# Kernel optimization log

Measured on AMD Instinct MI355X. Metric: run time of the kernel, lower is better.

## Reference

```python
import jax, jax.numpy as jnp
import numpy as np

N = 100_000      # nodes
E = 1_600_000    # edges
B = 256          # graphs
DIM = 64
EPS = 1e-5


def _batchnorm(h, gamma, beta):
    # BatchNorm1d in training mode: batch mean, biased variance
    mu = jnp.mean(h, axis=0)
    var = jnp.mean((h - mu) ** 2, axis=0)
    return (h - mu) * jax.lax.rsqrt(var + EPS) * gamma + beta


def setup_inputs() -> dict:
    key = jax.random.key(0)
    ks = jax.random.split(key, 12)
    x = jax.random.normal(ks[0], (N, DIM), dtype=jnp.float32)
    edge_index = jax.random.randint(ks[1], (2, E), 0, N, dtype=jnp.int64)
    edge_attr = jax.random.normal(ks[2], (E, DIM), dtype=jnp.float32)
    state = jax.random.normal(ks[3], (B, DIM), dtype=jnp.float32)
    batch = jnp.sort(jax.random.randint(ks[4], (N,), 0, B, dtype=jnp.int64))
    s = 0.05
    params = {
        "W1": jax.random.normal(ks[5], (DIM, 3 * DIM), dtype=jnp.float32) * s,
        "b1": jnp.zeros((DIM,), jnp.float32),
        "g1": jnp.ones((DIM,), jnp.float32),
        "be1": jnp.zeros((DIM,), jnp.float32),
        "W2": jax.random.normal(ks[6], (DIM, DIM), dtype=jnp.float32) * s,
        "b2": jnp.zeros((DIM,), jnp.float32),
        "g2": jnp.ones((DIM,), jnp.float32),
        "be2": jnp.zeros((DIM,), jnp.float32),
        "W3": jax.random.normal(ks[7], (DIM, DIM), dtype=jnp.float32) * s,
        "b3": jnp.zeros((DIM,), jnp.float32),
        "g3": jnp.ones((DIM,), jnp.float32),
        "be3": jnp.zeros((DIM,), jnp.float32),
    }
    return {"x": x, "edge_index": edge_index, "edge_attr": edge_attr,
            "state": state, "batch": batch, **params}


def reference(x, edge_index, edge_attr, state, batch,
              W1, b1, g1, be1, W2, b2, g2, be2, W3, b3, g3, be3):
    n = x.shape[0]
    src = edge_index[0]
    # scatter-mean of edge_attr onto destination-of-src nodes
    sums = jax.ops.segment_sum(edge_attr, src, num_segments=n)
    cnt = jax.ops.segment_sum(jnp.ones((edge_attr.shape[0],), edge_attr.dtype),
                              src, num_segments=n)
    v_mean = sums / jnp.maximum(cnt, 1.0)[:, None]
    comb = jnp.concatenate([x, v_mean, state[batch]], axis=1)  # [N, 3*DIM]
    h = jax.nn.relu(comb @ W1.T + b1)
    h = _batchnorm(h, g1, be1)
    h = jax.nn.relu(h @ W2.T + b2)
    h = _batchnorm(h, g2, be2)
    h = h @ W3.T + b3
    return _batchnorm(h, g3, be3)
```

## Files before the change

### kernel.cpp

```cpp
#include <hip/hip_runtime.h>

#define NN 100000
#define NE 1600000
#define EPSV 1e-5f

typedef float f32x4 __attribute__((ext_vector_type(4)));
typedef short s16x8 __attribute__((ext_vector_type(8)));

__device__ __forceinline__ unsigned short f2bf(float f) {
  unsigned int u = __float_as_uint(f);
  u += 0x7fffu + ((u >> 16) & 1u);
  return (unsigned short)(u >> 16);
}

__device__ __forceinline__ ushort4 pack4(float4 v) {
  ushort4 s;
  s.x = f2bf(v.x); s.y = f2bf(v.y); s.z = f2bf(v.z); s.w = f2bf(v.w);
  return s;
}

__global__ __launch_bounds__(256) void k_bucket(
    const int* __restrict__ ei, int* __restrict__ cnt, int* __restrict__ eids) {
  int e = blockIdx.x * 256 + threadIdx.x;
  int src = ei[e];
  int pos = atomicAdd(&cnt[src], 1);
  if (pos < 64) eids[(size_t)src * 64 + pos] = e;
}

__global__ __launch_bounds__(256) void k_gather(
    const int* __restrict__ cnt, const int* __restrict__ eids,
    const float* __restrict__ ea, float* __restrict__ vmean) {
  int n = __builtin_amdgcn_readfirstlane(blockIdx.x * 4 + (threadIdx.x >> 6));
  int lane = threadIdx.x & 63;
  const int* elist = eids + (size_t)n * 64;
  int c = cnt[n];
  int m = c < 64 ? c : 64;
  float a0 = 0.f, a1 = 0.f, a2 = 0.f, a3 = 0.f;
  int e = 0;
  for (; e + 4 <= m; e += 4) {
    int i0 = elist[e], i1 = elist[e + 1], i2 = elist[e + 2], i3 = elist[e + 3];
    a0 += ea[(size_t)i0 * 64 + lane];
    a1 += ea[(size_t)i1 * 64 + lane];
    a2 += ea[(size_t)i2 * 64 + lane];
    a3 += ea[(size_t)i3 * 64 + lane];
  }
  for (; e < m; ++e) a0 += ea[(size_t)elist[e] * 64 + lane];
  float inv = 1.0f / fmaxf((float)c, 1.0f);
  vmean[(size_t)n * 64 + lane] = (a0 + a1 + a2 + a3) * inv;
}

__global__ __launch_bounds__(256) void k_g1(
    const float4* __restrict__ x4, const float4* __restrict__ vmean4,
    const float4* __restrict__ state4,
    const int* __restrict__ batch, const float4* __restrict__ w14,
    const float* __restrict__ b1, unsigned short* __restrict__ h1,
    float* __restrict__ Sout, float* __restrict__ Qout) {
  __shared__ unsigned short lc[64][200];
  __shared__ unsigned short lw[64][200];
  __shared__ float ssum[64], ssq[64];
  const int tid = threadIdx.x;
  const int nodeBase = blockIdx.x * 64;
  if (tid < 64) { ssum[tid] = 0.f; ssq[tid] = 0.f; }
#pragma unroll
  for (int i = 0; i < 12; ++i) {
    int idx = tid + i * 256;
    int row = idx / 48, q = idx % 48;
    *(ushort4*)&lw[row][q * 4] = pack4(w14[idx]);
  }
#pragma unroll
  for (int i = 0; i < 4; ++i) {
    int idx = tid + i * 256;
    int node = idx >> 4, q = idx & 15;
    int g = nodeBase + node;
    float4 vx = {0,0,0,0}, vm = {0,0,0,0}, vs = {0,0,0,0};
    if (g < NN) {
      vx = x4[(size_t)g * 16 + q];
      vm = vmean4[(size_t)g * 16 + q];
      int b = batch[g];
      vs = state4[b * 16 + q];
    }
    *(ushort4*)&lc[node][q * 4]       = pack4(vx);
    *(ushort4*)&lc[node][64 + q * 4]  = pack4(vm);
    *(ushort4*)&lc[node][128 + q * 4] = pack4(vs);
  }
  __syncthreads();
  const int lane = tid & 63, w = tid >> 6;
  const int rg = lane >> 4, ci = lane & 15;
  f32x4 acc[4] = {{0,0,0,0},{0,0,0,0},{0,0,0,0},{0,0,0,0}};
#pragma unroll
  for (int s = 0; s < 6; ++s) {
    int k0 = 32 * s + rg * 8;
    s16x8 a = *(const s16x8*)&lc[w * 16 + ci][k0];
#pragma unroll
    for (int c = 0; c < 4; ++c) {
      s16x8 b = *(const s16x8*)&lw[c * 16 + ci][k0];
      acc[c] = __builtin_amdgcn_mfma_f32_16x16x32_bf16(a, b, acc[c], 0, 0, 0);
    }
  }
#pragma unroll
  for (int c = 0; c < 4; ++c) {
    int col = c * 16 + ci;
    float bb = b1[col];
    float ls = 0.f, lq = 0.f;
#pragma unroll
    for (int r = 0; r < 4; ++r) {
      int g = nodeBase + w * 16 + rg * 4 + r;
      if (g < NN) {
        float v = fmaxf(acc[c][r] + bb, 0.f);
        h1[(size_t)g * 64 + col] = f2bf(v);
        ls += v; lq += v * v;
      }
    }
    atomicAdd(&ssum[col], ls);
    atomicAdd(&ssq[col], lq);
  }
  __syncthreads();
  if (tid < 64) {
    unsafeAtomicAdd(&Sout[tid], ssum[tid]);
    unsafeAtomicAdd(&Qout[tid], ssq[tid]);
  }
}

template <bool RELU, bool OUTF32>
__global__ __launch_bounds__(256) void k_gemm64(
    const s16x8* __restrict__ A8,
    const float4* __restrict__ w4,
    const float* __restrict__ bias,
    const float* __restrict__ gm, const float* __restrict__ bt,
    const float* __restrict__ Sin, const float* __restrict__ Qin,
    unsigned short* __restrict__ Obf, float* __restrict__ Of32,
    float* __restrict__ Sout, float* __restrict__ Qout) {
  __shared__ unsigned short la[64][72];
  __shared__ unsigned short lwf[64][72];
  __shared__ float lA[64], lC[64], lD[64], ssum[64], ssq[64];
  const int tid = threadIdx.x;
  const int nodeBase = blockIdx.x * 64;
  if (tid < 64) {
    float mu = Sin[tid] * (1.0f / NN);
    float var = Qin[tid] * (1.0f / NN) - mu * mu;
    float a = gm[tid] * rsqrtf(var + EPSV);
    lA[tid] = a;
    lC[tid] = bt[tid] - mu * a;
    ssum[tid] = 0.f; ssq[tid] = 0.f;
  }
  __syncthreads();
#pragma unroll
  for (int i = 0; i < 2; ++i) {
    int idx = tid + i * 256;
    int row = idx >> 3, q = idx & 7;
    int g = nodeBase + row;
    s16x8 v = {};
    if (g < NN) v = A8[(size_t)g * 8 + q];
    *(s16x8*)&la[row][q * 8] = v;
  }
#pragma unroll
  for (int i = 0; i < 4; ++i) {
    int idx = tid + i * 256;
    int j = idx >> 4, q = idx & 15;
    float4 v = w4[idx];
    int k = q * 4;
    ushort4 s;
    s.x = f2bf(v.x * lA[k]);     s.y = f2bf(v.y * lA[k + 1]);
    s.z = f2bf(v.z * lA[k + 2]); s.w = f2bf(v.w * lA[k + 3]);
    *(ushort4*)&lwf[j][k] = s;
  }
  if (tid < 64) {
    const float* W = (const float*)w4 + tid * 64;
    float d = bias[tid];
    for (int k = 0; k < 64; ++k) d += lC[k] * W[k];
    lD[tid] = d;
  }
  __syncthreads();
  const int lane = tid & 63, w = tid >> 6;
  const int rg = lane >> 4, ci = lane & 15;
  f32x4 acc[4] = {{0,0,0,0},{0,0,0,0},{0,0,0,0},{0,0,0,0}};
#pragma unroll
  for (int s = 0; s < 2; ++s) {
    int k0 = 32 * s + rg * 8;
    s16x8 a = *(const s16x8*)&la[w * 16 + ci][k0];
#pragma unroll
    for (int c = 0; c < 4; ++c) {
      s16x8 b = *(const s16x8*)&lwf[c * 16 + ci][k0];
      acc[c] = __builtin_amdgcn_mfma_f32_16x16x32_bf16(a, b, acc[c], 0, 0, 0);
    }
  }
#pragma unroll
  for (int c = 0; c < 4; ++c) {
    int col = c * 16 + ci;
    float dd = lD[col];
    float ls = 0.f, lq = 0.f;
#pragma unroll
    for (int r = 0; r < 4; ++r) {
      int g = nodeBase + w * 16 + rg * 4 + r;
      if (g < NN) {
        float v = acc[c][r] + dd;
        if (RELU) v = fmaxf(v, 0.f);
        if (OUTF32) Of32[(size_t)g * 64 + col] = v;
        else        Obf[(size_t)g * 64 + col] = f2bf(v);
        ls += v; lq += v * v;
      }
    }
    atomicAdd(&ssum[col], ls);
    atomicAdd(&ssq[col], lq);
  }
  __syncthreads();
  if (tid < 64) {
    unsafeAtomicAdd(&Sout[tid], ssum[tid]);
    unsafeAtomicAdd(&Qout[tid], ssq[tid]);
  }
}

__global__ __launch_bounds__(256) void k_bn3(
    const float4* __restrict__ h3, const float* __restrict__ gm,
    const float* __restrict__ bt, const float* __restrict__ S,
    const float* __restrict__ Q, float4* __restrict__ out) {
  __shared__ float lA[64], lC[64];
  const int tid = threadIdx.x;
  if (tid < 64) {
    float mu = S[tid] * (1.0f / NN);
    float var = Q[tid] * (1.0f / NN) - mu * mu;
    float a = gm[tid] * rsqrtf(var + EPSV);
    lA[tid] = a;
    lC[tid] = bt[tid] - mu * a;
  }
  __syncthreads();
  const int total = NN * 16;
  for (int idx = blockIdx.x * 256 + tid; idx < total; idx += gridDim.x * 256) {
    float4 v = h3[idx];
    int k = (idx & 15) * 4;
    v.x = v.x * lA[k]     + lC[k];
    v.y = v.y * lA[k + 1] + lC[k + 1];
    v.z = v.z * lA[k + 2] + lC[k + 2];
    v.w = v.w * lA[k + 3] + lC[k + 3];
    out[idx] = v;
  }
}

extern "C" void kernel_launch(void* const* d_in, const int* in_sizes, int n_in,
                              void* d_out, int out_size, void* d_ws, size_t ws_size,
                              hipStream_t stream) {
  const float* x     = (const float*)d_in[0];
  const int*   ei    = (const int*)d_in[1];
  const float* ea    = (const float*)d_in[2];
  const float* state = (const float*)d_in[3];
  const int*   batch = (const int*)d_in[4];
  const float* W1  = (const float*)d_in[5];
  const float* b1  = (const float*)d_in[6];
  const float* g1  = (const float*)d_in[7];
  const float* be1 = (const float*)d_in[8];
  const float* W2  = (const float*)d_in[9];
  const float* b2  = (const float*)d_in[10];
  const float* g2  = (const float*)d_in[11];
  const float* be2 = (const float*)d_in[12];
  const float* W3  = (const float*)d_in[13];
  const float* b3  = (const float*)d_in[14];
  const float* g3  = (const float*)d_in[15];
  const float* be3 = (const float*)d_in[16];

  char* ws = (char*)d_ws;
  int*   cnt  = (int*)ws;
  float* S1   = (float*)(ws + 400000);
  float* Q1 = S1 + 64;
  float* S2 = S1 + 128;
  float* Q2 = S1 + 192;
  float* S3 = S1 + 256;
  float* Q3 = S1 + 320;
  int*            eids  = (int*)(ws + 401536);
  float*          h3    = (float*)(ws + 401536);
  float*          vmean = (float*)(ws + 26001536);
  unsigned short* h2    = (unsigned short*)(ws + 26001536);
  unsigned short* h1    = (unsigned short*)(ws + 51601536);

  hipMemsetAsync(ws, 0, 401536, stream);

  k_bucket<<<NE / 256, 256, 0, stream>>>(ei, cnt, eids);
  k_gather<<<NN / 4, 256, 0, stream>>>(cnt, eids, ea, vmean);

  const int nblk = (NN + 63) / 64;
  k_g1<<<nblk, 256, 0, stream>>>((const float4*)x, (const float4*)vmean,
                                 (const float4*)state, batch, (const float4*)W1,
                                 b1, h1, S1, Q1);
  k_gemm64<true, false><<<nblk, 256, 0, stream>>>(
      (const s16x8*)h1, (const float4*)W2, b2, g1, be1, S1, Q1, h2, nullptr, S2, Q2);
  k_gemm64<false, true><<<nblk, 256, 0, stream>>>(
      (const s16x8*)h2, (const float4*)W3, b3, g2, be2, S2, Q2, nullptr, h3, S3, Q3);
  k_bn3<<<2048, 256, 0, stream>>>((const float4*)h3, g3, be3, S3, Q3, (float4*)d_out);
}
```

Measured before the change: 399.5 us.

## Vectorize gather, store intermediates as bf16, stage outputs in LDS, precompute folded weights

The edge gather now uses float4 loads with four edge groups per wave and a shuffle reduction, and stores the mean in bf16. GEMM outputs go through LDS so global stores are 16-byte coalesced, and h3 is kept in bf16 to halve its traffic. BatchNorm folding of W2/W3 moves into a single-block prep kernel instead of being redone in every block. In exchange there are two extra serial launches and more bf16 rounding in vmean and h3.

```diff
diff --git a/kernel.cpp b/kernel.cpp
--- a/kernel.cpp
+++ b/kernel.cpp
@@ -11,6 +11,10 @@
   unsigned int u = __float_as_uint(f);
   u += 0x7fffu + ((u >> 16) & 1u);
   return (unsigned short)(u >> 16);
+}
+
+__device__ __forceinline__ float bf2f(unsigned short s) {
+  return __uint_as_float(((unsigned int)s) << 16);
 }
 
 __device__ __forceinline__ ushort4 pack4(float4 v) {
@@ -29,28 +33,45 @@
 
 __global__ __launch_bounds__(256) void k_gather(
     const int* __restrict__ cnt, const int* __restrict__ eids,
-    const float* __restrict__ ea, float* __restrict__ vmean) {
+    const float4* __restrict__ ea4, ushort4* __restrict__ vmb4) {
   int n = __builtin_amdgcn_readfirstlane(blockIdx.x * 4 + (threadIdx.x >> 6));
   int lane = threadIdx.x & 63;
+  int grp = lane >> 4, q = lane & 15;
   const int* elist = eids + (size_t)n * 64;
   int c = cnt[n];
   int m = c < 64 ? c : 64;
-  float a0 = 0.f, a1 = 0.f, a2 = 0.f, a3 = 0.f;
-  int e = 0;
-  for (; e + 4 <= m; e += 4) {
-    int i0 = elist[e], i1 = elist[e + 1], i2 = elist[e + 2], i3 = elist[e + 3];
-    a0 += ea[(size_t)i0 * 64 + lane];
-    a1 += ea[(size_t)i1 * 64 + lane];
-    a2 += ea[(size_t)i2 * 64 + lane];
-    a3 += ea[(size_t)i3 * 64 + lane];
-  }
-  for (; e < m; ++e) a0 += ea[(size_t)elist[e] * 64 + lane];
-  float inv = 1.0f / fmaxf((float)c, 1.0f);
-  vmean[(size_t)n * 64 + lane] = (a0 + a1 + a2 + a3) * inv;
+  float ax = 0.f, ay = 0.f, az = 0.f, aw = 0.f;
+  for (int e = 0; e < m; e += 16) {
+    int rm = m - 1;
+    int r0 = e + grp, r1 = e + 4 + grp, r2 = e + 8 + grp, r3 = e + 12 + grp;
+    int i0 = elist[r0 < m ? r0 : rm];
+    int i1 = elist[r1 < m ? r1 : rm];
+    int i2 = elist[r2 < m ? r2 : rm];
+    int i3 = elist[r3 < m ? r3 : rm];
+    float4 v0 = ea4[(size_t)i0 * 16 + q];
+    float4 v1 = ea4[(size_t)i1 * 16 + q];
+    float4 v2 = ea4[(size_t)i2 * 16 + q];
+    float4 v3 = ea4[(size_t)i3 * 16 + q];
+    float m0 = r0 < m ? 1.f : 0.f, m1 = r1 < m ? 1.f : 0.f;
+    float m2 = r2 < m ? 1.f : 0.f, m3 = r3 < m ? 1.f : 0.f;
+    ax += m0 * v0.x + m1 * v1.x + m2 * v2.x + m3 * v3.x;
+    ay += m0 * v0.y + m1 * v1.y + m2 * v2.y + m3 * v3.y;
+    az += m0 * v0.z + m1 * v1.z + m2 * v2.z + m3 * v3.z;
+    aw += m0 * v0.w + m1 * v1.w + m2 * v2.w + m3 * v3.w;
+  }
+  ax += __shfl_xor(ax, 16); ay += __shfl_xor(ay, 16);
+  az += __shfl_xor(az, 16); aw += __shfl_xor(aw, 16);
+  ax += __shfl_xor(ax, 32); ay += __shfl_xor(ay, 32);
+  az += __shfl_xor(az, 32); aw += __shfl_xor(aw, 32);
+  if (lane < 16) {
+    float inv = 1.0f / fmaxf((float)c, 1.0f);
+    float4 r; r.x = ax * inv; r.y = ay * inv; r.z = az * inv; r.w = aw * inv;
+    vmb4[(size_t)n * 16 + lane] = pack4(r);
+  }
 }
 
 __global__ __launch_bounds__(256) void k_g1(
-    const float4* __restrict__ x4, const float4* __restrict__ vmean4,
+    const float4* __restrict__ x4, const ushort4* __restrict__ vmb4,
     const float4* __restrict__ state4,
     const int* __restrict__ batch, const float4* __restrict__ w14,
     const float* __restrict__ b1, unsigned short* __restrict__ h1,
@@ -72,15 +93,16 @@
     int idx = tid + i * 256;
     int node = idx >> 4, q = idx & 15;
     int g = nodeBase + node;
-    float4 vx = {0,0,0,0}, vm = {0,0,0,0}, vs = {0,0,0,0};
+    float4 vx = {0,0,0,0}, vs = {0,0,0,0};
+    ushort4 vm = {0,0,0,0};
     if (g < NN) {
       vx = x4[(size_t)g * 16 + q];
-      vm = vmean4[(size_t)g * 16 + q];
+      vm = vmb4[(size_t)g * 16 + q];
       int b = batch[g];
       vs = state4[b * 16 + q];
     }
     *(ushort4*)&lc[node][q * 4]       = pack4(vx);
-    *(ushort4*)&lc[node][64 + q * 4]  = pack4(vm);
+    *(ushort4*)&lc[node][64 + q * 4]  = vm;
     *(ushort4*)&lc[node][128 + q * 4] = pack4(vs);
   }
   __syncthreads();
@@ -97,6 +119,8 @@
       acc[c] = __builtin_amdgcn_mfma_f32_16x16x32_bf16(a, b, acc[c], 0, 0, 0);
     }
   }
+  __syncthreads();
+  unsigned short (*lo)[72] = (unsigned short(*)[72])lw;
 #pragma unroll
   for (int c = 0; c < 4; ++c) {
     int col = c * 16 + ci;
@@ -104,46 +128,71 @@
     float ls = 0.f, lq = 0.f;
 #pragma unroll
     for (int r = 0; r < 4; ++r) {
-      int g = nodeBase + w * 16 + rg * 4 + r;
-      if (g < NN) {
-        float v = fmaxf(acc[c][r] + bb, 0.f);
-        h1[(size_t)g * 64 + col] = f2bf(v);
-        ls += v; lq += v * v;
-      }
+      int row = w * 16 + rg * 4 + r;
+      float v = fmaxf(acc[c][r] + bb, 0.f);
+      lo[row][col] = f2bf(v);
+      if (nodeBase + row < NN) { ls += v; lq += v * v; }
     }
     atomicAdd(&ssum[col], ls);
     atomicAdd(&ssq[col], lq);
   }
   __syncthreads();
+#pragma unroll
+  for (int i = 0; i < 2; ++i) {
+    int idx = tid + i * 256;
+    int row = idx >> 3, q = idx & 7;
+    int g = nodeBase + row;
+    if (g < NN) *(s16x8*)&h1[(size_t)g * 64 + q * 8] = *(const s16x8*)&lo[row][q * 8];
+  }
   if (tid < 64) {
     unsafeAtomicAdd(&Sout[tid], ssum[tid]);
     unsafeAtomicAdd(&Qout[tid], ssq[tid]);
   }
 }
 
-template <bool RELU, bool OUTF32>
+__global__ __launch_bounds__(256) void k_prep(
+    const float* __restrict__ Sin, const float* __restrict__ Qin,
+    const float* __restrict__ gm, const float* __restrict__ bt,
+    const float* __restrict__ W, const float* __restrict__ bias,
+    unsigned short* __restrict__ wf, float* __restrict__ dout) {
+  __shared__ float lA[64], lC[64], red[256];
+  int t = threadIdx.x;
+  if (t < 64) {
+    float mu = Sin[t] * (1.0f / NN);
+    float var = Qin[t] * (1.0f / NN) - mu * mu;
+    float a = gm[t] * rsqrtf(var + EPSV);
+    lA[t] = a;
+    lC[t] = bt[t] - mu * a;
+  }
+  __syncthreads();
+#pragma unroll
+  for (int i = 0; i < 16; ++i) {
+    int idx = t + i * 256;
+    wf[idx] = f2bf(W[idx] * lA[idx & 63]);
+  }
+  int j = t >> 2, p = t & 3;
+  const float* Wr = W + j * 64 + p * 16;
+  float s = 0.f;
+#pragma unroll
+  for (int k = 0; k < 16; ++k) s += lC[p * 16 + k] * Wr[k];
+  red[t] = s;
+  __syncthreads();
+  if (t < 64) dout[t] = bias[t] + red[t * 4] + red[t * 4 + 1] + red[t * 4 + 2] + red[t * 4 + 3];
+}
+
+template <bool RELU>
 __global__ __launch_bounds__(256) void k_gemm64(
     const s16x8* __restrict__ A8,
-    const float4* __restrict__ w4,
-    const float* __restrict__ bias,
-    const float* __restrict__ gm, const float* __restrict__ bt,
-    const float* __restrict__ Sin, const float* __restrict__ Qin,
-    unsigned short* __restrict__ Obf, float* __restrict__ Of32,
+    const s16x8* __restrict__ w8,
+    const float* __restrict__ d,
+    unsigned short* __restrict__ Obf,
     float* __restrict__ Sout, float* __restrict__ Qout) {
   __shared__ unsigned short la[64][72];
   __shared__ unsigned short lwf[64][72];
-  __shared__ float lA[64], lC[64], lD[64], ssum[64], ssq[64];
+  __shared__ float ssum[64], ssq[64];
   const int tid = threadIdx.x;
   const int nodeBase = blockIdx.x * 64;
-  if (tid < 64) {
-    float mu = Sin[tid] * (1.0f / NN);
-    float var = Qin[tid] * (1.0f / NN) - mu * mu;
-    float a = gm[tid] * rsqrtf(var + EPSV);
-    lA[tid] = a;
-    lC[tid] = bt[tid] - mu * a;
-    ssum[tid] = 0.f; ssq[tid] = 0.f;
-  }
-  __syncthreads();
+  if (tid < 64) { ssum[tid] = 0.f; ssq[tid] = 0.f; }
 #pragma unroll
   for (int i = 0; i < 2; ++i) {
     int idx = tid + i * 256;
@@ -154,21 +203,10 @@
     *(s16x8*)&la[row][q * 8] = v;
   }
 #pragma unroll
-  for (int i = 0; i < 4; ++i) {
-    int idx = tid + i * 256;
-    int j = idx >> 4, q = idx & 15;
-    float4 v = w4[idx];
-    int k = q * 4;
-    ushort4 s;
-    s.x = f2bf(v.x * lA[k]);     s.y = f2bf(v.y * lA[k + 1]);
-    s.z = f2bf(v.z * lA[k + 2]); s.w = f2bf(v.w * lA[k + 3]);
-    *(ushort4*)&lwf[j][k] = s;
-  }
-  if (tid < 64) {
-    const float* W = (const float*)w4 + tid * 64;
-    float d = bias[tid];
-    for (int k = 0; k < 64; ++k) d += lC[k] * W[k];
-    lD[tid] = d;
+  for (int i = 0; i < 2; ++i) {
+    int idx = tid + i * 256;
+    int j = idx >> 3, q = idx & 7;
+    *(s16x8*)&lwf[j][q * 8] = w8[idx];
   }
   __syncthreads();
   const int lane = tid & 63, w = tid >> 6;
@@ -184,26 +222,32 @@
       acc[c] = __builtin_amdgcn_mfma_f32_16x16x32_bf16(a, b, acc[c], 0, 0, 0);
     }
   }
+  __syncthreads();
+  unsigned short (*lo)[72] = (unsigned short(*)[72])la;
 #pragma unroll
   for (int c = 0; c < 4; ++c) {
     int col = c * 16 + ci;
-    float dd = lD[col];
+    float dd = d[col];
     float ls = 0.f, lq = 0.f;
 #pragma unroll
     for (int r = 0; r < 4; ++r) {
-      int g = nodeBase + w * 16 + rg * 4 + r;
-      if (g < NN) {
-        float v = acc[c][r] + dd;
-        if (RELU) v = fmaxf(v, 0.f);
-        if (OUTF32) Of32[(size_t)g * 64 + col] = v;
-        else        Obf[(size_t)g * 64 + col] = f2bf(v);
-        ls += v; lq += v * v;
-      }
+      int row = w * 16 + rg * 4 + r;
+      float v = acc[c][r] + dd;
+      if (RELU) v = fmaxf(v, 0.f);
+      lo[row][col] = f2bf(v);
+      if (nodeBase + row < NN) { ls += v; lq += v * v; }
     }
     atomicAdd(&ssum[col], ls);
     atomicAdd(&ssq[col], lq);
   }
   __syncthreads();
+#pragma unroll
+  for (int i = 0; i < 2; ++i) {
+    int idx = tid + i * 256;
+    int row = idx >> 3, q = idx & 7;
+    int g = nodeBase + row;
+    if (g < NN) *(s16x8*)&Obf[(size_t)g * 64 + q * 8] = *(const s16x8*)&lo[row][q * 8];
+  }
   if (tid < 64) {
     unsafeAtomicAdd(&Sout[tid], ssum[tid]);
     unsafeAtomicAdd(&Qout[tid], ssq[tid]);
@@ -211,7 +255,7 @@
 }
 
 __global__ __launch_bounds__(256) void k_bn3(
-    const float4* __restrict__ h3, const float* __restrict__ gm,
+    const s16x8* __restrict__ h3b, const float* __restrict__ gm,
     const float* __restrict__ bt, const float* __restrict__ S,
     const float* __restrict__ Q, float4* __restrict__ out) {
   __shared__ float lA[64], lC[64];
@@ -224,15 +268,21 @@
     lC[tid] = bt[tid] - mu * a;
   }
   __syncthreads();
-  const int total = NN * 16;
+  const int total = NN * 8;
   for (int idx = blockIdx.x * 256 + tid; idx < total; idx += gridDim.x * 256) {
-    float4 v = h3[idx];
-    int k = (idx & 15) * 4;
-    v.x = v.x * lA[k]     + lC[k];
-    v.y = v.y * lA[k + 1] + lC[k + 1];
-    v.z = v.z * lA[k + 2] + lC[k + 2];
-    v.w = v.w * lA[k + 3] + lC[k + 3];
-    out[idx] = v;
+    s16x8 v = h3b[idx];
+    int k = (idx & 7) * 8;
+    float4 o0, o1;
+    o0.x = bf2f((unsigned short)v[0]) * lA[k]     + lC[k];
+    o0.y = bf2f((unsigned short)v[1]) * lA[k + 1] + lC[k + 1];
+    o0.z = bf2f((unsigned short)v[2]) * lA[k + 2] + lC[k + 2];
+    o0.w = bf2f((unsigned short)v[3]) * lA[k + 3] + lC[k + 3];
+    o1.x = bf2f((unsigned short)v[4]) * lA[k + 4] + lC[k + 4];
+    o1.y = bf2f((unsigned short)v[5]) * lA[k + 5] + lC[k + 5];
+    o1.z = bf2f((unsigned short)v[6]) * lA[k + 6] + lC[k + 6];
+    o1.w = bf2f((unsigned short)v[7]) * lA[k + 7] + lC[k + 7];
+    out[idx * 2]     = o0;
+    out[idx * 2 + 1] = o1;
   }
 }
 
@@ -241,7 +291,6 @@
                               hipStream_t stream) {
   const float* x     = (const float*)d_in[0];
   const int*   ei    = (const int*)d_in[1];
-  const float* ea    = (const float*)d_in[2];
   const float* state = (const float*)d_in[3];
   const int*   batch = (const int*)d_in[4];
   const float* W1  = (const float*)d_in[5];
@@ -256,6 +305,7 @@
   const float* b3  = (const float*)d_in[14];
   const float* g3  = (const float*)d_in[15];
   const float* be3 = (const float*)d_in[16];
+  const float* ea  = (const float*)d_in[2];
 
   char* ws = (char*)d_ws;
   int*   cnt  = (int*)ws;
@@ -265,24 +315,30 @@
   float* Q2 = S1 + 192;
   float* S3 = S1 + 256;
   float* Q3 = S1 + 320;
-  int*            eids  = (int*)(ws + 401536);
-  float*          h3    = (float*)(ws + 401536);
-  float*          vmean = (float*)(ws + 26001536);
-  unsigned short* h2    = (unsigned short*)(ws + 26001536);
-  unsigned short* h1    = (unsigned short*)(ws + 51601536);
+  unsigned short* w2f = (unsigned short*)(ws + 401536);
+  float*          d2  = (float*)(ws + 409728);
+  unsigned short* w3f = (unsigned short*)(ws + 409984);
+  float*          d3  = (float*)(ws + 418176);
+  int*            eids = (int*)(ws + 418432);
+  unsigned short* h3b  = (unsigned short*)(ws + 418432);
+  unsigned short* vmb  = (unsigned short*)(ws + 26018432);
+  unsigned short* h2   = (unsigned short*)(ws + 26018432);
+  unsigned short* h1   = (unsigned short*)(ws + 38818432);
 
   hipMemsetAsync(ws, 0, 401536, stream);
 
   k_bucket<<<NE / 256, 256, 0, stream>>>(ei, cnt, eids);
-  k_gather<<<NN / 4, 256, 0, stream>>>(cnt, eids, ea, vmean);
+  k_gather<<<NN / 4, 256, 0, stream>>>(cnt, eids, (const float4*)ea, (ushort4*)vmb);
 
   const int nblk = (NN + 63) / 64;
-  k_g1<<<nblk, 256, 0, stream>>>((const float4*)x, (const float4*)vmean,
+  k_g1<<<nblk, 256, 0, stream>>>((const float4*)x, (const ushort4*)vmb,
                                  (const float4*)state, batch, (const float4*)W1,
                                  b1, h1, S1, Q1);
-  k_gemm64<true, false><<<nblk, 256, 0, stream>>>(
-      (const s16x8*)h1, (const float4*)W2, b2, g1, be1, S1, Q1, h2, nullptr, S2, Q2);
-  k_gemm64<false, true><<<nblk, 256, 0, stream>>>(
-      (const s16x8*)h2, (const float4*)W3, b3, g2, be2, S2, Q2, nullptr, h3, S3, Q3);
-  k_bn3<<<2048, 256, 0, stream>>>((const float4*)h3, g3, be3, S3, Q3, (float4*)d_out);
-}
+  k_prep<<<1, 256, 0, stream>>>(S1, Q1, g1, be1, W2, b2, w2f, d2);
+  k_gemm64<true><<<nblk, 256, 0, stream>>>(
+      (const s16x8*)h1, (const s16x8*)w2f, d2, h2, S2, Q2);
+  k_prep<<<1, 256, 0, stream>>>(S2, Q2, g2, be2, W3, b3, w3f, d3);
+  k_gemm64<false><<<nblk, 256, 0, stream>>>(
+      (const s16x8*)h2, (const s16x8*)w3f, d3, h3b, S3, Q3);
+  k_bn3<<<2048, 256, 0, stream>>>((const s16x8*)h3b, g3, be3, S3, Q3, (float4*)d_out);
+}
```

After: 385.7 us. -3.5%, faster.
